# Performance work log

Measured on AMD Instinct MI355X. Metric: run time of the kernel, lower is better.

The kernel has to match this reference:

```python
import jax, jax.numpy as jnp
import numpy as np

N = 50000   # nodes per graph
E = 800000  # edges per graph (even, message() splits in half)
F = 100     # node/edge feature dim (init_count_size / init_emb_size)
D = 64      # hidden_dim3 = rule_graph_dim
W_SCALE = 0.05


def _mlp(x, w1, b1, w2, b2):
    return jax.nn.relu(x @ w1 + b1) @ w2 + b2


def _triple_conv(x, src, dst, ea, lw, lb, l2w, l2b, nn_fn):
    # PyG flow source_to_target: x_j = x[edge_index[0]], x_i = x[edge_index[1]]
    h = ea.shape[0] // 2
    x_j = x[src]
    x_i = x[dst]
    m1 = jax.nn.relu(jnp.concatenate([x_i[:h], ea[:h], x_j[:h]], 1) @ lw + lb)
    m2 = jax.nn.relu(jnp.concatenate([x_j[h:], ea[h:], x_i[h:]], 1) @ l2w + l2b)
    msgs = jnp.concatenate([m1, m2], 0)
    agg = jax.ops.segment_sum(msgs, dst, num_segments=x.shape[0])
    # eps = 0.0 buffer -> out = agg + (1+eps)*x = agg + x
    return nn_fn(agg + x)


def setup_inputs() -> dict:
    key = jax.random.key(0)
    ks = jax.random.split(key, 32)
    inp = {
        'features_1': jax.random.normal(ks[0], (N, F), jnp.float32),
        'edge_index_1': jax.random.randint(ks[1], (2, E), 0, N, jnp.int64 if jax.config.jax_enable_x64 else jnp.int32).astype(jnp.int32),
        'edge_attr_1': jax.random.normal(ks[2], (E, F), jnp.float32),
        'features_2': jax.random.normal(ks[3], (N, F), jnp.float32),
        'edge_index_2': jax.random.randint(ks[4], (2, E), 0, N, jnp.int32),
        'edge_attr_2': jax.random.normal(ks[5], (E, F), jnp.float32),
        'c1_lin_w': jax.random.normal(ks[6], (3 * F, F), jnp.float32) * W_SCALE,
        'c1_lin_b': jax.random.normal(ks[7], (F,), jnp.float32) * W_SCALE,
        'c1_lin2_w': jax.random.normal(ks[8], (3 * F, F), jnp.float32) * W_SCALE,
        'c1_lin2_b': jax.random.normal(ks[9], (F,), jnp.float32) * W_SCALE,
        'mlp1_w1': jax.random.normal(ks[10], (F, F), jnp.float32) * W_SCALE,
        'mlp1_b1': jax.random.normal(ks[11], (F,), jnp.float32) * W_SCALE,
        'mlp1_w2': jax.random.normal(ks[12], (F, F), jnp.float32) * W_SCALE,
        'mlp1_b2': jax.random.normal(ks[13], (F,), jnp.float32) * W_SCALE,
        'c2_lin_w': jax.random.normal(ks[14], (3 * F, F), jnp.float32) * W_SCALE,
        'c2_lin_b': jax.random.normal(ks[15], (F,), jnp.float32) * W_SCALE,
        'c2_lin2_w': jax.random.normal(ks[16], (3 * F, F), jnp.float32) * W_SCALE,
        'c2_lin2_b': jax.random.normal(ks[17], (F,), jnp.float32) * W_SCALE,
        'mlp2_w1': jax.random.normal(ks[18], (F, D), jnp.float32) * W_SCALE,
        'mlp2_b1': jax.random.normal(ks[19], (D,), jnp.float32) * W_SCALE,
        'mlp2_w2': jax.random.normal(ks[20], (D, D), jnp.float32) * W_SCALE,
        'mlp2_b2': jax.random.normal(ks[21], (D,), jnp.float32) * W_SCALE,
    }
    return inp


def reference(features_1, edge_index_1, edge_attr_1,
              features_2, edge_index_2, edge_attr_2,
              c1_lin_w, c1_lin_b, c1_lin2_w, c1_lin2_b,
              mlp1_w1, mlp1_b1, mlp1_w2, mlp1_b2,
              c2_lin_w, c2_lin_b, c2_lin2_w, c2_lin2_b,
              mlp2_w1, mlp2_b1, mlp2_w2, mlp2_b2):

    def conv_pass(x, ei, ea):
        src, dst = ei[0], ei[1]
        x = _triple_conv(x, src, dst, ea, c1_lin_w, c1_lin_b, c1_lin2_w, c1_lin2_b,
                         lambda z: _mlp(z, mlp1_w1, mlp1_b1, mlp1_w2, mlp1_b2))
        x = jax.nn.relu(x)
        x = _triple_conv(x, src, dst, ea, c2_lin_w, c2_lin_b, c2_lin2_w, c2_lin2_b,
                         lambda z: _mlp(z, mlp2_w1, mlp2_b1, mlp2_w2, mlp2_b2))
        return x

    f1 = conv_pass(features_1, edge_index_1, edge_attr_1)  # [N, D]
    f2 = conv_pass(features_2, edge_index_2, edge_attr_2)  # [N, D]
    # global_add_pool with a single batch id -> sum over nodes
    g1 = jnp.sum(f1, axis=0)
    g2 = jnp.sum(f2, axis=0)
    return jnp.stack([g1, g2], 0)  # [2, D]
```

## Files before the change

kernel.cpp:

```cpp
#include <hip/hip_runtime.h>

#define F 100
#define TS 256

typedef __attribute__((ext_vector_type(4))) unsigned short us4;
typedef __attribute__((ext_vector_type(8))) short short8;
typedef __attribute__((ext_vector_type(4))) float f32x4;

static __device__ __forceinline__ unsigned short f2bf(float f) {
    unsigned int u = __float_as_uint(f);
    unsigned int r = (u + 0x7FFF + ((u >> 16) & 1)) >> 16;
    return (unsigned short)r;
}
static __device__ __forceinline__ float bf2f(unsigned short u) {
    return __uint_as_float(((unsigned int)u) << 16);
}

__global__ __launch_bounds__(TS)
void hist2_kernel(const int* __restrict__ dst0, const int* __restrict__ dst1,
                  int h, int E, int N,
                  int* __restrict__ cnt1, int* __restrict__ cnt2)
{
    for (int idx = blockIdx.x * TS + threadIdx.x; idx < 2 * E; idx += gridDim.x * TS) {
        int g = idx >= E;
        int e = idx - g * E;
        int d = (g ? dst1 : dst0)[e];
        atomicAdd((e < h ? cnt1 : cnt2) + g * N + d, 1);
    }
}

__global__ __launch_bounds__(1024)
void scan4_kernel(const int* __restrict__ cnt1, const int* __restrict__ cnt2,
                  int* __restrict__ rp1, int* __restrict__ rp2, int n)
{
    const int which = blockIdx.x;
    const int hf = which >> 1, g = which & 1;
    const int* cnt = (hf ? cnt2 : cnt1) + g * n;
    int* rp = (hf ? rp2 : rp1) + g * (n + 1);
    __shared__ int buf[1024];
    __shared__ int carry_s;
    const int t = threadIdx.x;
    if (t == 0) carry_s = 0;
    __syncthreads();
    for (int base = 0; base < n; base += 8192) {
        int v[8], s = 0;
        #pragma unroll
        for (int j = 0; j < 8; ++j) {
            int idx = base + t * 8 + j;
            int x = (idx < n) ? cnt[idx] : 0;
            v[j] = s; s += x;
        }
        buf[t] = s;
        __syncthreads();
        for (int off = 1; off < 1024; off <<= 1) {
            int y = (t >= off) ? buf[t - off] : 0;
            __syncthreads();
            buf[t] += y;
            __syncthreads();
        }
        int excl = carry_s + buf[t] - s;
        #pragma unroll
        for (int j = 0; j < 8; ++j) {
            int idx = base + t * 8 + j;
            if (idx < n) rp[idx] = excl + v[j];
        }
        __syncthreads();
        if (t == 1023) carry_s += buf[1023];
        __syncthreads();
    }
    if (t == 0) rp[n] = carry_s;
}

__global__ __launch_bounds__(TS)
void scatter2_kernel(const int* __restrict__ src0, const int* __restrict__ dst0,
                     const int* __restrict__ src1, const int* __restrict__ dst1,
                     int h, int E, int N,
                     const int* __restrict__ rp1, const int* __restrict__ rp2,
                     int* __restrict__ cur1, int* __restrict__ cur2,
                     int* __restrict__ perm1, int* __restrict__ perm2,
                     int* __restrict__ es1, int* __restrict__ es2)
{
    for (int idx = blockIdx.x * TS + threadIdx.x; idx < 2 * E; idx += gridDim.x * TS) {
        int g = idx >= E;
        int e = idx - g * E;
        int d = (g ? dst1 : dst0)[e];
        int s = (g ? src1 : src0)[e];
        if (e < h) {
            int p = rp1[g * (N + 1) + d] + atomicAdd(&cur1[g * N + d], 1);
            perm1[g * h + p] = e; es1[g * h + p] = s + g * N;
        } else {
            int p = rp2[g * (N + 1) + d] + atomicAdd(&cur2[g * N + d], 1);
            perm2[g * h + p] = e; es2[g * h + p] = s + g * N;
        }
    }
}

__global__ __launch_bounds__(TS)
void pack_w_kernel(const float* w0, const float* w1, const float* w2, const float* w3,
                   unsigned short* __restrict__ Wp)
{
    int i = blockIdx.x * TS + threadIdx.x;
    if (i >= 12 * 112 * 128) return;
    int s = i / (112 * 128);
    int r = i - s * (112 * 128);
    int c = r >> 7, k = r & 127;
    int wi = s & 3, grp = s >> 2;
    const float* w = (wi == 0) ? w0 : (wi == 1) ? w1 : (wi == 2) ? w2 : w3;
    int off = (grp == 0) ? F : ((grp == 1) ? 0 : 2 * F);
    unsigned short v = 0;
    if (c < 100 && k < 100) v = f2bf(w[(off + k) * F + c]);
    Wp[i] = v;
}

__global__ __launch_bounds__(TS)
void pack_w2_kernel(const float* __restrict__ w, int K, int Nc, int ldb,
                    unsigned short* __restrict__ out)
{
    int i = blockIdx.x * TS + threadIdx.x;
    if (i >= 112 * 128) return;
    int c = i >> 7, k = i & 127;
    unsigned short v = 0;
    if (c < Nc && k < K) v = f2bf(w[k * ldb + c]);
    out[i] = v;
}

__global__ __launch_bounds__(TS)
void pack_x2_kernel(const float* __restrict__ x0, const float* __restrict__ x1,
                    int N, unsigned short* __restrict__ xb)
{
    const size_t total = (size_t)N * 2 * 32;
    for (size_t i = (size_t)blockIdx.x * TS + threadIdx.x; i < total; i += (size_t)gridDim.x * TS) {
        int n = (int)(i >> 5), q = (int)(i & 31);
        int g = n >= N;
        const float* x = g ? x1 : x0;
        int nl = n - g * N;
        us4 o = (us4){0, 0, 0, 0};
        if (q < 25) {
            float4 v = *(const float4*)&x[(size_t)nl * 100 + q * 4];
            o.x = f2bf(v.x); o.y = f2bf(v.y); o.z = f2bf(v.z); o.w = f2bf(v.w);
        }
        *(us4*)&xb[((size_t)n << 7) + q * 4] = o;
    }
}

__global__ __launch_bounds__(TS)
void pack_sum2_f32(const float* __restrict__ agg,
                   const float* __restrict__ x0, const float* __restrict__ x1,
                   int N, unsigned short* __restrict__ Ab)
{
    const size_t total = (size_t)N * 2 * 32;
    for (size_t i = (size_t)blockIdx.x * TS + threadIdx.x; i < total; i += (size_t)gridDim.x * TS) {
        int n = (int)(i >> 5), q = (int)(i & 31);
        int g = n >= N;
        const float* x = g ? x1 : x0;
        int nl = n - g * N;
        us4 o = (us4){0, 0, 0, 0};
        if (q < 25) {
            float4 a = *(const float4*)&agg[(size_t)n * 100 + q * 4];
            float4 v = *(const float4*)&x[(size_t)nl * 100 + q * 4];
            o.x = f2bf(a.x + v.x); o.y = f2bf(a.y + v.y);
            o.z = f2bf(a.z + v.z); o.w = f2bf(a.w + v.w);
        }
        *(us4*)&Ab[((size_t)n << 7) + q * 4] = o;
    }
}

__global__ __launch_bounds__(TS)
void pack_sum_bf16(const float* __restrict__ agg, const unsigned short* __restrict__ xb,
                   int M, unsigned short* __restrict__ Ab)
{
    const size_t total = (size_t)M * 32;
    for (size_t i = (size_t)blockIdx.x * TS + threadIdx.x; i < total; i += (size_t)gridDim.x * TS) {
        int n = (int)(i >> 5), q = (int)(i & 31);
        us4 o = (us4){0, 0, 0, 0};
        if (q < 25) {
            float4 a = *(const float4*)&agg[(size_t)n * 100 + q * 4];
            us4 v = *(const us4*)&xb[((size_t)n << 7) + q * 4];
            o.x = f2bf(a.x + bf2f(v.x)); o.y = f2bf(a.y + bf2f(v.y));
            o.z = f2bf(a.z + bf2f(v.z)); o.w = f2bf(a.w + bf2f(v.w));
        }
        *(us4*)&Ab[((size_t)n << 7) + q * 4] = o;
    }
}

__global__ __launch_bounds__(TS)
void gemm_node_mfma(const unsigned short* __restrict__ xb,
                    const unsigned short* __restrict__ B0, const unsigned short* __restrict__ B1,
                    const unsigned short* __restrict__ B2, const unsigned short* __restrict__ B3,
                    unsigned short* __restrict__ NTb,
                    int M)
{
    const int t = threadIdx.x, lane = t & 63, wv = t >> 6;
    const int rA = lane & 15, kg = lane >> 4;
    const unsigned short* Bp[4] = {B0, B1, B2, B3};
    const int ntiles = (M + 15) >> 4;
    for (int tile = blockIdx.x * 4 + wv; tile < ntiles; tile += gridDim.x * 4) {
        const int base = tile << 4;
        const int arow = min(base + rA, M - 1);
        short8 A[4];
        #pragma unroll
        for (int ks = 0; ks < 4; ++ks)
            A[ks] = *(const short8*)&xb[((size_t)arow << 7) + ks * 32 + kg * 8];
        const int row = base + rA;
        #pragma unroll
        for (int sel = 0; sel < 4; ++sel) {
            const unsigned short* B = Bp[sel];
            f32x4 C[7];
            #pragma unroll
            for (int nf = 0; nf < 7; ++nf) C[nf] = (f32x4){0.f, 0.f, 0.f, 0.f};
            #pragma unroll
            for (int ks = 0; ks < 4; ++ks) {
                #pragma unroll
                for (int nf = 0; nf < 7; ++nf) {
                    short8 Bf = *(const short8*)&B[(size_t)(rA + nf * 16) * 128 + ks * 32 + kg * 8];
                    C[nf] = __builtin_amdgcn_mfma_f32_16x16x32_bf16(Bf, A[ks], C[nf], 0, 0, 0);
                }
            }
            if (row < M) {
                #pragma unroll
                for (int nf = 0; nf < 7; ++nf) {
                    const int cb = nf * 16 + kg * 4;
                    if (cb < 100) {
                        us4 o;
                        o.x = f2bf(C[nf][0]); o.y = f2bf(C[nf][1]);
                        o.z = f2bf(C[nf][2]); o.w = f2bf(C[nf][3]);
                        *(us4*)&NTb[(size_t)row * 400 + sel * 100 + cb] = o;
                    }
                }
            }
        }
    }
}

__global__ __launch_bounds__(TS)
void gemm_edge_quad(const float* __restrict__ ea0, const float* __restrict__ ea1,
                    const int* __restrict__ perm,
                    const unsigned short* __restrict__ W0,
                    const unsigned short* __restrict__ W1,
                    unsigned short* __restrict__ P0,
                    unsigned short* __restrict__ P1,
                    int h)
{
    __shared__ unsigned short sA[2][64][136];
    const int t = threadIdx.x, lane = t & 63, wv = t >> 6;
    const int rA = lane & 15, kg = lane >> 4;
    const int M = 2 * h;
    const int ngrp = M >> 6;
    const int r_loc = t >> 2, sub = t & 3;

    int grp = blockIdx.x;
    if (grp >= ngrp) return;

    {
        const int grow = (grp << 6) + r_loc;
        const int g = grow >= h;
        const int e = perm[grow];
        const float* ea = (g ? ea1 : ea0) + (size_t)e * 100;
        float4 raw[7];
        #pragma unroll
        for (int j = 0; j < 7; ++j) {
            const int q = sub + 4 * j;
            if (q < 25) raw[j] = *(const float4*)&ea[q * 4];
        }
        #pragma unroll
        for (int j = 0; j < 8; ++j) {
            const int q = sub + 4 * j;
            us4 o = (us4){0, 0, 0, 0};
            if (j < 7 && q < 25) {
                o.x = f2bf(raw[j].x); o.y = f2bf(raw[j].y);
                o.z = f2bf(raw[j].z); o.w = f2bf(raw[j].w);
            }
            if (q < 32) *(us4*)&sA[0][r_loc][q * 4] = o;
        }
    }
    __syncthreads();

    int cur = 0;
    while (true) {
        const int nxt = grp + gridDim.x;
        const bool more = nxt < ngrp;

        float4 raw[7];
        if (more) {
            const int grow = (nxt << 6) + r_loc;
            const int g = grow >= h;
            const int e = perm[grow];
            const float* ea = (g ? ea1 : ea0) + (size_t)e * 100;
            #pragma unroll
            for (int j = 0; j < 7; ++j) {
                const int q = sub + 4 * j;
                if (q < 25) raw[j] = *(const float4*)&ea[q * 4];
            }
        }

        {
            const int lrow = wv * 16 + rA;
            short8 A[4];
            #pragma unroll
            for (int ks = 0; ks < 4; ++ks)
                A[ks] = *(const short8*)&sA[cur][lrow][ks * 32 + kg * 8];

            f32x4 C0[7], C1[7];
            #pragma unroll
            for (int nf = 0; nf < 7; ++nf) {
                C0[nf] = (f32x4){0.f, 0.f, 0.f, 0.f};
                C1[nf] = (f32x4){0.f, 0.f, 0.f, 0.f};
            }
            #pragma unroll
            for (int ks = 0; ks < 4; ++ks) {
                #pragma unroll
                for (int nf = 0; nf < 7; ++nf) {
                    short8 B0f = *(const short8*)&W0[(size_t)(rA + nf * 16) * 128 + ks * 32 + kg * 8];
                    C0[nf] = __builtin_amdgcn_mfma_f32_16x16x32_bf16(B0f, A[ks], C0[nf], 0, 0, 0);
                    short8 B1f = *(const short8*)&W1[(size_t)(rA + nf * 16) * 128 + ks * 32 + kg * 8];
                    C1[nf] = __builtin_amdgcn_mfma_f32_16x16x32_bf16(B1f, A[ks], C1[nf], 0, 0, 0);
                }
            }
            const int row = (grp << 6) + lrow;
            #pragma unroll
            for (int nf = 0; nf < 7; ++nf) {
                const int cb = nf * 16 + kg * 4;
                if (cb < 100) {
                    us4 o0, o1;
                    o0.x = f2bf(C0[nf][0]); o0.y = f2bf(C0[nf][1]);
                    o0.z = f2bf(C0[nf][2]); o0.w = f2bf(C0[nf][3]);
                    o1.x = f2bf(C1[nf][0]); o1.y = f2bf(C1[nf][1]);
                    o1.z = f2bf(C1[nf][2]); o1.w = f2bf(C1[nf][3]);
                    *(us4*)&P0[(size_t)row * 100 + cb] = o0;
                    *(us4*)&P1[(size_t)row * 100 + cb] = o1;
                }
            }
        }

        if (!more) break;

        #pragma unroll
        for (int j = 0; j < 8; ++j) {
            const int q = sub + 4 * j;
            us4 o = (us4){0, 0, 0, 0};
            if (j < 7 && q < 25) {
                o.x = f2bf(raw[j].x); o.y = f2bf(raw[j].y);
                o.z = f2bf(raw[j].z); o.w = f2bf(raw[j].w);
            }
            if (q < 32) *(us4*)&sA[cur ^ 1][r_loc][q * 4] = o;
        }
        __syncthreads();
        cur ^= 1; grp = nxt;
    }
}

__global__ __launch_bounds__(TS)
void seg_reduce_both(const unsigned short* __restrict__ PA,
                     const unsigned short* __restrict__ PB,
                     const int* __restrict__ es1, const int* __restrict__ es2,
                     const int* __restrict__ rp1, const int* __restrict__ rp2,
                     const float* __restrict__ cb, const float* __restrict__ cb2,
                     const unsigned short* __restrict__ NTb,
                     float* __restrict__ agg,
                     int N, int h)
{
    const int gid = blockIdx.x * TS + threadIdx.x;
    const int n = gid >> 5, q = gid & 31;
    if (n >= 2 * N || q >= 25) return;
    const int c4 = q * 4;
    const int g = n >= N;
    const int nl = n - g * N;

    float ax = 0.f, ay = 0.f, az = 0.f, aw = 0.f;

    {
        const us4 vd = *(const us4*)&NTb[(size_t)n * 400 + 0 * 100 + c4];
        const float4 bi = *(const float4*)&cb[c4];
        const float dx = bf2f(vd.x) + bi.x, dy = bf2f(vd.y) + bi.y;
        const float dz = bf2f(vd.z) + bi.z, dw = bf2f(vd.w) + bi.w;
        const int* rpg = rp1 + g * (N + 1);
        int p0 = max(rpg[nl], 0) + g * h;
        int p1 = min(rpg[nl + 1], h) + g * h;
        for (int pos = p0; pos < p1; ++pos) {
            const int s = es1[pos];
            const us4 pv = *(const us4*)&PA[(size_t)pos * 100 + c4];
            const us4 vs = *(const us4*)&NTb[(size_t)s * 400 + 1 * 100 + c4];
            ax += fmaxf(bf2f(pv.x) + bf2f(vs.x) + dx, 0.f);
            ay += fmaxf(bf2f(pv.y) + bf2f(vs.y) + dy, 0.f);
            az += fmaxf(bf2f(pv.z) + bf2f(vs.z) + dz, 0.f);
            aw += fmaxf(bf2f(pv.w) + bf2f(vs.w) + dw, 0.f);
        }
    }
    {
        const us4 vd = *(const us4*)&NTb[(size_t)n * 400 + 3 * 100 + c4];
        const float4 bi = *(const float4*)&cb2[c4];
        const float dx = bf2f(vd.x) + bi.x, dy = bf2f(vd.y) + bi.y;
        const float dz = bf2f(vd.z) + bi.z, dw = bf2f(vd.w) + bi.w;
        const int* rpg = rp2 + g * (N + 1);
        int p0 = max(rpg[nl], 0) + g * h;
        int p1 = min(rpg[nl + 1], h) + g * h;
        for (int pos = p0; pos < p1; ++pos) {
            const int s = es2[pos];
            const us4 pv = *(const us4*)&PB[(size_t)pos * 100 + c4];
            const us4 vs = *(const us4*)&NTb[(size_t)s * 400 + 2 * 100 + c4];
            ax += fmaxf(bf2f(pv.x) + bf2f(vs.x) + dx, 0.f);
            ay += fmaxf(bf2f(pv.y) + bf2f(vs.y) + dy, 0.f);
            az += fmaxf(bf2f(pv.z) + bf2f(vs.z) + dz, 0.f);
            aw += fmaxf(bf2f(pv.w) + bf2f(vs.w) + dw, 0.f);
        }
    }
    float* ap = &agg[(size_t)n * 100 + c4];
    ap[0] = ax; ap[1] = ay; ap[2] = az; ap[3] = aw;
}

__global__ __launch_bounds__(TS)
void gemm_mlp_bf16out(const unsigned short* __restrict__ Ab,
                      const unsigned short* __restrict__ Wp,
                      const float* __restrict__ bias,
                      unsigned short* __restrict__ out,
                      int M, int Nc)
{
    const int t = threadIdx.x, lane = t & 63, wv = t >> 6;
    const int rA = lane & 15, kg = lane >> 4;
    const int ntiles = (M + 15) >> 4;
    for (int tile = blockIdx.x * 4 + wv; tile < ntiles; tile += gridDim.x * 4) {
        const int base = tile << 4;
        const int arow = min(base + rA, M - 1);
        f32x4 C[7];
        #pragma unroll
        for (int nf = 0; nf < 7; ++nf) C[nf] = (f32x4){0.f, 0.f, 0.f, 0.f};
        #pragma unroll
        for (int ks = 0; ks < 4; ++ks) {
            short8 A = *(const short8*)&Ab[((size_t)arow << 7) + ks * 32 + kg * 8];
            #pragma unroll
            for (int nf = 0; nf < 7; ++nf) {
                short8 B = *(const short8*)&Wp[(size_t)(rA + nf * 16) * 128 + ks * 32 + kg * 8];
                C[nf] = __builtin_amdgcn_mfma_f32_16x16x32_bf16(B, A, C[nf], 0, 0, 0);
            }
        }
        const int row = base + rA;
        if (row < M) {
            #pragma unroll
            for (int nf = 0; nf < 7; ++nf) {
                const int cb = nf * 16 + kg * 4;
                us4 o = (us4){0, 0, 0, 0};
                if (cb < Nc) {
                    float4 bv = *(const float4*)&bias[cb];
                    o.x = f2bf(fmaxf(C[nf][0] + bv.x, 0.f));
                    o.y = f2bf(fmaxf(C[nf][1] + bv.y, 0.f));
                    o.z = f2bf(fmaxf(C[nf][2] + bv.z, 0.f));
                    o.w = f2bf(fmaxf(C[nf][3] + bv.w, 0.f));
                }
                *(us4*)&out[((size_t)row << 7) + cb] = o;
            }
            *(us4*)&out[((size_t)row << 7) + 112 + kg * 4] = (us4){0, 0, 0, 0};
        }
    }
}

__global__ __launch_bounds__(TS)
void gemm_mlp_f32out(const unsigned short* __restrict__ Ab,
                     const unsigned short* __restrict__ Wp,
                     const float* __restrict__ bias,
                     float* __restrict__ out,
                     int M)
{
    const int t = threadIdx.x, lane = t & 63, wv = t >> 6;
    const int rA = lane & 15, kg = lane >> 4;
    const int ntiles = (M + 15) >> 4;
    for (int tile = blockIdx.x * 4 + wv; tile < ntiles; tile += gridDim.x * 4) {
        const int base = tile << 4;
        const int arow = min(base + rA, M - 1);
        f32x4 C[4];
        #pragma unroll
        for (int nf = 0; nf < 4; ++nf) C[nf] = (f32x4){0.f, 0.f, 0.f, 0.f};
        #pragma unroll
        for (int ks = 0; ks < 2; ++ks) {
            short8 A = *(const short8*)&Ab[((size_t)arow << 7) + ks * 32 + kg * 8];
            #pragma unroll
            for (int nf = 0; nf < 4; ++nf) {
                short8 B = *(const short8*)&Wp[(size_t)(rA + nf * 16) * 128 + ks * 32 + kg * 8];
                C[nf] = __builtin_amdgcn_mfma_f32_16x16x32_bf16(B, A, C[nf], 0, 0, 0);
            }
        }
        const int row = base + rA;
        if (row < M) {
            #pragma unroll
            for (int nf = 0; nf < 4; ++nf) {
                const int cb = nf * 16 + kg * 4;
                float4 bv = *(const float4*)&bias[cb];
                float4 o;
                o.x = C[nf][0] + bv.x; o.y = C[nf][1] + bv.y;
                o.z = C[nf][2] + bv.z; o.w = C[nf][3] + bv.w;
                *(float4*)&out[(size_t)row * 64 + cb] = o;
            }
        }
    }
}

__global__ __launch_bounds__(TS)
void colsum2_kernel(const float* __restrict__ Fm, int N, float* __restrict__ out)
{
    __shared__ float red[4][2][64];
    const int t = threadIdx.x;
    const int c = t & 63, rg = t >> 6;
    float s0 = 0.f, s1 = 0.f;
    const int M = 2 * N;
    for (int r = blockIdx.x * 4 + rg; r < M; r += gridDim.x * 4) {
        float v = Fm[(size_t)r * 64 + c];
        if (r < N) s0 += v; else s1 += v;
    }
    red[rg][0][c] = s0; red[rg][1][c] = s1;
    __syncthreads();
    if (rg == 0) {
        atomicAdd(&out[c],      red[0][0][c] + red[1][0][c] + red[2][0][c] + red[3][0][c]);
        atomicAdd(&out[64 + c], red[0][1][c] + red[1][1][c] + red[2][1][c] + red[3][1][c]);
    }
}

extern "C" void kernel_launch(void* const* d_in, const int* in_sizes, int n_in,
                              void* d_out, int out_size, void* d_ws, size_t ws_size,
                              hipStream_t stream)
{
    const int N = in_sizes[0] / F;
    const int E = in_sizes[1] / 2;
    const int h = E / 2;
    const int N2 = 2 * N, h2 = 2 * h;

    unsigned short* NTb  = (unsigned short*)d_ws;
    float* AGG = (float*)(NTb + (size_t)N2 * 400);
    unsigned short* P1A = (unsigned short*)(AGG + (size_t)N2 * 100);
    unsigned short* P1B = P1A + (size_t)h2 * 100;
    unsigned short* P2A = P1B + (size_t)h2 * 100;
    unsigned short* P2B = P2A + (size_t)h2 * 100;
    unsigned short* xb  = P2B + (size_t)h2 * 100;
    unsigned short* X1b = xb + (size_t)N2 * 128;
    unsigned short* Ab  = X1b + (size_t)N2 * 128;
    unsigned short* Hb  = Ab + (size_t)N2 * 128;
    int* rp1   = (int*)(Hb + (size_t)N2 * 128);
    int* rp2   = rp1 + 2 * (N + 1);
    int* cnt1  = rp2 + 2 * (N + 1);
    int* cnt2  = cnt1 + N2;
    int* perm1 = cnt2 + N2;
    int* perm2 = perm1 + h2;
    int* es1   = perm2 + h2;
    int* es2   = es1 + h2;
    unsigned short* Wp = (unsigned short*)(es2 + h2);
    unsigned short* Wm = Wp + (size_t)12 * 112 * 128;
    float* F2 = AGG;

    const float* x0g0 = (const float*)d_in[0];
    const int*   ei0  = (const int*)d_in[1];
    const float* ea0  = (const float*)d_in[2];
    const float* x0g1 = (const float*)d_in[3];
    const int*   ei1  = (const int*)d_in[4];
    const float* ea1  = (const float*)d_in[5];
    const float* c1w  = (const float*)d_in[6];
    const float* c1b  = (const float*)d_in[7];
    const float* c1w2 = (const float*)d_in[8];
    const float* c1b2 = (const float*)d_in[9];
    const float* m1w1 = (const float*)d_in[10];
    const float* m1b1 = (const float*)d_in[11];
    const float* m1w2 = (const float*)d_in[12];
    const float* m1b2 = (const float*)d_in[13];
    const float* c2w  = (const float*)d_in[14];
    const float* c2b  = (const float*)d_in[15];
    const float* c2w2 = (const float*)d_in[16];
    const float* c2b2 = (const float*)d_in[17];
    const float* m2w1 = (const float*)d_in[18];
    const float* m2b1 = (const float*)d_in[19];
    const float* m2w2 = (const float*)d_in[20];
    const float* m2b2 = (const float*)d_in[21];

    hipMemsetAsync(d_out, 0, (size_t)out_size * sizeof(float), stream);

    const dim3 blk(TS);
    const size_t SL = (size_t)112 * 128;
    pack_w_kernel<<<(12 * 112 * 128 + TS - 1) / TS, blk, 0, stream>>>(c1w, c1w2, c2w, c2w2, Wp);
    pack_w2_kernel<<<56, blk, 0, stream>>>(m1w1, 100, 100, 100, Wm + 0 * SL);
    pack_w2_kernel<<<56, blk, 0, stream>>>(m1w2, 100, 100, 100, Wm + 1 * SL);
    pack_w2_kernel<<<56, blk, 0, stream>>>(m2w1, 100,  64,  64, Wm + 2 * SL);
    pack_w2_kernel<<<56, blk, 0, stream>>>(m2w2,  64,  64,  64, Wm + 3 * SL);

    hipMemsetAsync(cnt1, 0, 2 * (size_t)N2 * sizeof(int), stream);
    hist2_kernel<<<2048, blk, 0, stream>>>(ei0 + E, ei1 + E, h, E, N, cnt1, cnt2);
    scan4_kernel<<<4, 1024, 0, stream>>>(cnt1, cnt2, rp1, rp2, N);
    hipMemsetAsync(cnt1, 0, 2 * (size_t)N2 * sizeof(int), stream);
    scatter2_kernel<<<2048, blk, 0, stream>>>(ei0, ei0 + E, ei1, ei1 + E, h, E, N,
                                              rp1, rp2, cnt1, cnt2, perm1, perm2, es1, es2);
    pack_x2_kernel<<<2048, blk, 0, stream>>>(x0g0, x0g1, N, xb);

    gemm_edge_quad<<<2048, blk, 0, stream>>>(ea0, ea1, perm1,
                                             Wp + 0 * SL, Wp + 2 * SL, P1A, P2A, h);
    gemm_edge_quad<<<2048, blk, 0, stream>>>(ea0, ea1, perm2,
                                             Wp + 1 * SL, Wp + 3 * SL, P1B, P2B, h);

    const int nblkR = (N2 * 32 + TS - 1) / TS;
    for (int conv = 0; conv < 2; ++conv) {
        const float* cb  = conv ? c2b  : c1b;
        const float* cb2 = conv ? c2b2 : c1b2;
        const unsigned short* xin = conv ? X1b : xb;
        const int iw  = conv ? 2 : 0;
        const int iw2 = conv ? 3 : 1;
        const unsigned short* PA = conv ? P2A : P1A;
        const unsigned short* PB = conv ? P2B : P1B;

        gemm_node_mfma<<<2048, blk, 0, stream>>>(xin,
            Wp + (size_t)(4 + iw)  * SL, Wp + (size_t)(8 + iw)  * SL,
            Wp + (size_t)(4 + iw2) * SL, Wp + (size_t)(8 + iw2) * SL,
            NTb, N2);

        seg_reduce_both<<<nblkR, blk, 0, stream>>>(PA, PB, es1, es2, rp1, rp2,
                                                   cb, cb2, NTb, AGG, N, h);

        if (conv == 0) {
            pack_sum2_f32<<<2048, blk, 0, stream>>>(AGG, x0g0, x0g1, N, Ab);
            gemm_mlp_bf16out<<<2048, blk, 0, stream>>>(Ab, Wm + 0 * SL, m1b1, Hb,  N2, 100);
            gemm_mlp_bf16out<<<2048, blk, 0, stream>>>(Hb, Wm + 1 * SL, m1b2, X1b, N2, 100);
        } else {
            pack_sum_bf16<<<2048, blk, 0, stream>>>(AGG, X1b, N2, Ab);
            gemm_mlp_bf16out<<<2048, blk, 0, stream>>>(Ab, Wm + 2 * SL, m2b1, Hb, N2, 64);
            gemm_mlp_f32out<<<2048, blk, 0, stream>>>(Hb, Wm + 3 * SL, m2b2, F2, N2);
        }
    }
    colsum2_kernel<<<512, blk, 0, stream>>>(F2, N, (float*)d_out);
    (void)ws_size; (void)n_in;
}
```

Before: 1.463 ms.

## Fuse edge-attr GEMM with segment reduction per node block using LDS atomics

Replaces the precomputed bf16 edge-projection buffers and the separate segment-reduce kernel with one kernel per conv. Each block owns a range of 40 destination nodes, runs the edge_attr MFMA GEMM on its CSR-sorted edges, adds the source and destination node terms and the bias, applies ReLU, and accumulates into LDS with atomics before writing agg. This removes the large intermediate P buffers and their write/read traffic. In exchange it recomputes the edge GEMM per conv, rereads edge_attr twice, and adds LDS atomic contention plus load imbalance across node blocks.

New measurement: 2.278 ms. 55.7% more time.

```diff
diff --git a/kernel.cpp b/kernel.cpp
--- a/kernel.cpp
+++ b/kernel.cpp
@@ -2,6 +2,7 @@
 
 #define F 100
 #define TS 256
+#define NPB 40
 
 typedef __attribute__((ext_vector_type(4))) unsigned short us4;
 typedef __attribute__((ext_vector_type(8))) short short8;
@@ -78,7 +79,8 @@
                      const int* __restrict__ rp1, const int* __restrict__ rp2,
                      int* __restrict__ cur1, int* __restrict__ cur2,
                      int* __restrict__ perm1, int* __restrict__ perm2,
-                     int* __restrict__ es1, int* __restrict__ es2)
+                     int* __restrict__ es1, int* __restrict__ es2,
+                     int* __restrict__ ds1, int* __restrict__ ds2)
 {
     for (int idx = blockIdx.x * TS + threadIdx.x; idx < 2 * E; idx += gridDim.x * TS) {
         int g = idx >= E;
@@ -87,10 +89,10 @@
         int s = (g ? src1 : src0)[e];
         if (e < h) {
             int p = rp1[g * (N + 1) + d] + atomicAdd(&cur1[g * N + d], 1);
-            perm1[g * h + p] = e; es1[g * h + p] = s + g * N;
+            perm1[g * h + p] = e; es1[g * h + p] = s + g * N; ds1[g * h + p] = d + g * N;
         } else {
             int p = rp2[g * (N + 1) + d] + atomicAdd(&cur2[g * N + d], 1);
-            perm2[g * h + p] = e; es2[g * h + p] = s + g * N;
+            perm2[g * h + p] = e; es2[g * h + p] = s + g * N; ds2[g * h + p] = d + g * N;
         }
     }
 }
@@ -233,179 +235,165 @@
 }
 
 __global__ __launch_bounds__(TS)
-void gemm_edge_quad(const float* __restrict__ ea0, const float* __restrict__ ea1,
-                    const int* __restrict__ perm,
-                    const unsigned short* __restrict__ W0,
-                    const unsigned short* __restrict__ W1,
-                    unsigned short* __restrict__ P0,
-                    unsigned short* __restrict__ P1,
-                    int h)
-{
+void fused_edge_conv(const float* __restrict__ ea0, const float* __restrict__ ea1,
+                     const int* __restrict__ perm1, const int* __restrict__ es1, const int* __restrict__ ds1,
+                     const int* __restrict__ perm2, const int* __restrict__ es2, const int* __restrict__ ds2,
+                     const int* __restrict__ rp1, const int* __restrict__ rp2,
+                     const unsigned short* __restrict__ WA, const unsigned short* __restrict__ WB,
+                     const float* __restrict__ cbA, const float* __restrict__ cbB,
+                     const unsigned short* __restrict__ NTb,
+                     float* __restrict__ agg,
+                     int N, int h, int cpg)
+{
+    __shared__ float aggL[NPB][104];
     __shared__ unsigned short sA[2][64][136];
+
     const int t = threadIdx.x, lane = t & 63, wv = t >> 6;
     const int rA = lane & 15, kg = lane >> 4;
-    const int M = 2 * h;
-    const int ngrp = M >> 6;
     const int r_loc = t >> 2, sub = t & 3;
 
-    int grp = blockIdx.x;
-    if (grp >= ngrp) return;
-
-    {
-        const int grow = (grp << 6) + r_loc;
-        const int g = grow >= h;
-        const int e = perm[grow];
-        const float* ea = (g ? ea1 : ea0) + (size_t)e * 100;
-        float4 raw[7];
-        #pragma unroll
-        for (int j = 0; j < 7; ++j) {
-            const int q = sub + 4 * j;
-            if (q < 25) raw[j] = *(const float4*)&ea[q * 4];
-        }
-        #pragma unroll
-        for (int j = 0; j < 8; ++j) {
-            const int q = sub + 4 * j;
-            us4 o = (us4){0, 0, 0, 0};
-            if (j < 7 && q < 25) {
-                o.x = f2bf(raw[j].x); o.y = f2bf(raw[j].y);
-                o.z = f2bf(raw[j].z); o.w = f2bf(raw[j].w);
-            }
-            if (q < 32) *(us4*)&sA[0][r_loc][q * 4] = o;
-        }
-    }
-    __syncthreads();
-
-    int cur = 0;
-    while (true) {
-        const int nxt = grp + gridDim.x;
-        const bool more = nxt < ngrp;
-
-        float4 raw[7];
-        if (more) {
-            const int grow = (nxt << 6) + r_loc;
-            const int g = grow >= h;
-            const int e = perm[grow];
-            const float* ea = (g ? ea1 : ea0) + (size_t)e * 100;
+    const int b = blockIdx.x;
+    const int g = b >= cpg;
+    const int ci = b - g * cpg;
+    const int n0 = g * N + ci * NPB;
+    const int n1 = min(n0 + NPB, (g + 1) * N);
+    const int nrows = n1 - n0;
+    if (nrows <= 0) return;
+
+    for (int i = t; i < NPB * 104; i += TS) ((float*)aggL)[i] = 0.f;
+
+    const float* eaG = g ? ea1 : ea0;
+
+    #pragma unroll 1
+    for (int ph = 0; ph < 2; ++ph) {
+        const int* rp   = (ph ? rp2 : rp1) + g * (N + 1);
+        const int* perm = ph ? perm2 : perm1;
+        const int* es   = ph ? es2 : es1;
+        const int* ds   = ph ? ds2 : ds1;
+        const unsigned short* W = ph ? WB : WA;
+        const float* cbp = ph ? cbB : cbA;
+        const int seld = ph ? 3 : 0;
+        const int sels = ph ? 2 : 1;
+
+        const int nl0 = n0 - g * N;
+        const int p_lo = rp[nl0] + g * h;
+        const int p_hi = rp[nl0 + nrows] + g * h;
+        if (p_lo >= p_hi) continue;
+
+        float bv[7];
+        #pragma unroll
+        for (int nf = 0; nf < 7; ++nf) {
+            const int c = rA + nf * 16;
+            bv[nf] = (c < 100) ? cbp[c] : 0.f;
+        }
+
+        __syncthreads();
+        {
+            const int pos0 = min(p_lo + r_loc, p_hi - 1);
+            const int e = perm[pos0];
+            const float* er = eaG + (size_t)e * 100;
+            float4 raw[7];
             #pragma unroll
             for (int j = 0; j < 7; ++j) {
                 const int q = sub + 4 * j;
-                if (q < 25) raw[j] = *(const float4*)&ea[q * 4];
-            }
-        }
-
-        {
-            const int lrow = wv * 16 + rA;
-            short8 A[4];
-            #pragma unroll
-            for (int ks = 0; ks < 4; ++ks)
-                A[ks] = *(const short8*)&sA[cur][lrow][ks * 32 + kg * 8];
-
-            f32x4 C0[7], C1[7];
-            #pragma unroll
-            for (int nf = 0; nf < 7; ++nf) {
-                C0[nf] = (f32x4){0.f, 0.f, 0.f, 0.f};
-                C1[nf] = (f32x4){0.f, 0.f, 0.f, 0.f};
-            }
-            #pragma unroll
-            for (int ks = 0; ks < 4; ++ks) {
+                if (q < 25) raw[j] = *(const float4*)&er[q * 4];
+            }
+            #pragma unroll
+            for (int j = 0; j < 8; ++j) {
+                const int q = sub + 4 * j;
+                us4 o = (us4){0, 0, 0, 0};
+                if (j < 7 && q < 25) {
+                    o.x = f2bf(raw[j].x); o.y = f2bf(raw[j].y);
+                    o.z = f2bf(raw[j].z); o.w = f2bf(raw[j].w);
+                }
+                *(us4*)&sA[0][r_loc][q * 4] = o;
+            }
+        }
+        __syncthreads();
+
+        int gb = p_lo, cur = 0;
+        while (true) {
+            const int nb = gb + 64;
+            const bool more = nb < p_hi;
+
+            float4 raw[7];
+            if (more) {
+                const int pos0 = min(nb + r_loc, p_hi - 1);
+                const int e = perm[pos0];
+                const float* er = eaG + (size_t)e * 100;
                 #pragma unroll
-                for (int nf = 0; nf < 7; ++nf) {
-                    short8 B0f = *(const short8*)&W0[(size_t)(rA + nf * 16) * 128 + ks * 32 + kg * 8];
-                    C0[nf] = __builtin_amdgcn_mfma_f32_16x16x32_bf16(B0f, A[ks], C0[nf], 0, 0, 0);
-                    short8 B1f = *(const short8*)&W1[(size_t)(rA + nf * 16) * 128 + ks * 32 + kg * 8];
-                    C1[nf] = __builtin_amdgcn_mfma_f32_16x16x32_bf16(B1f, A[ks], C1[nf], 0, 0, 0);
-                }
-            }
-            const int row = (grp << 6) + lrow;
-            #pragma unroll
-            for (int nf = 0; nf < 7; ++nf) {
-                const int cb = nf * 16 + kg * 4;
-                if (cb < 100) {
-                    us4 o0, o1;
-                    o0.x = f2bf(C0[nf][0]); o0.y = f2bf(C0[nf][1]);
-                    o0.z = f2bf(C0[nf][2]); o0.w = f2bf(C0[nf][3]);
-                    o1.x = f2bf(C1[nf][0]); o1.y = f2bf(C1[nf][1]);
-                    o1.z = f2bf(C1[nf][2]); o1.w = f2bf(C1[nf][3]);
-                    *(us4*)&P0[(size_t)row * 100 + cb] = o0;
-                    *(us4*)&P1[(size_t)row * 100 + cb] = o1;
-                }
-            }
-        }
-
-        if (!more) break;
-
-        #pragma unroll
-        for (int j = 0; j < 8; ++j) {
-            const int q = sub + 4 * j;
-            us4 o = (us4){0, 0, 0, 0};
-            if (j < 7 && q < 25) {
-                o.x = f2bf(raw[j].x); o.y = f2bf(raw[j].y);
-                o.z = f2bf(raw[j].z); o.w = f2bf(raw[j].w);
-            }
-            if (q < 32) *(us4*)&sA[cur ^ 1][r_loc][q * 4] = o;
-        }
-        __syncthreads();
-        cur ^= 1; grp = nxt;
-    }
-}
-
-__global__ __launch_bounds__(TS)
-void seg_reduce_both(const unsigned short* __restrict__ PA,
-                     const unsigned short* __restrict__ PB,
-                     const int* __restrict__ es1, const int* __restrict__ es2,
-                     const int* __restrict__ rp1, const int* __restrict__ rp2,
-                     const float* __restrict__ cb, const float* __restrict__ cb2,
-                     const unsigned short* __restrict__ NTb,
-                     float* __restrict__ agg,
-                     int N, int h)
-{
-    const int gid = blockIdx.x * TS + threadIdx.x;
-    const int n = gid >> 5, q = gid & 31;
-    if (n >= 2 * N || q >= 25) return;
-    const int c4 = q * 4;
-    const int g = n >= N;
-    const int nl = n - g * N;
-
-    float ax = 0.f, ay = 0.f, az = 0.f, aw = 0.f;
-
-    {
-        const us4 vd = *(const us4*)&NTb[(size_t)n * 400 + 0 * 100 + c4];
-        const float4 bi = *(const float4*)&cb[c4];
-        const float dx = bf2f(vd.x) + bi.x, dy = bf2f(vd.y) + bi.y;
-        const float dz = bf2f(vd.z) + bi.z, dw = bf2f(vd.w) + bi.w;
-        const int* rpg = rp1 + g * (N + 1);
-        int p0 = max(rpg[nl], 0) + g * h;
-        int p1 = min(rpg[nl + 1], h) + g * h;
-        for (int pos = p0; pos < p1; ++pos) {
-            const int s = es1[pos];
-            const us4 pv = *(const us4*)&PA[(size_t)pos * 100 + c4];
-            const us4 vs = *(const us4*)&NTb[(size_t)s * 400 + 1 * 100 + c4];
-            ax += fmaxf(bf2f(pv.x) + bf2f(vs.x) + dx, 0.f);
-            ay += fmaxf(bf2f(pv.y) + bf2f(vs.y) + dy, 0.f);
-            az += fmaxf(bf2f(pv.z) + bf2f(vs.z) + dz, 0.f);
-            aw += fmaxf(bf2f(pv.w) + bf2f(vs.w) + dw, 0.f);
-        }
-    }
-    {
-        const us4 vd = *(const us4*)&NTb[(size_t)n * 400 + 3 * 100 + c4];
-        const float4 bi = *(const float4*)&cb2[c4];
-        const float dx = bf2f(vd.x) + bi.x, dy = bf2f(vd.y) + bi.y;
-        const float dz = bf2f(vd.z) + bi.z, dw = bf2f(vd.w) + bi.w;
-        const int* rpg = rp2 + g * (N + 1);
-        int p0 = max(rpg[nl], 0) + g * h;
-        int p1 = min(rpg[nl + 1], h) + g * h;
-        for (int pos = p0; pos < p1; ++pos) {
-            const int s = es2[pos];
-            const us4 pv = *(const us4*)&PB[(size_t)pos * 100 + c4];
-            const us4 vs = *(const us4*)&NTb[(size_t)s * 400 + 2 * 100 + c4];
-            ax += fmaxf(bf2f(pv.x) + bf2f(vs.x) + dx, 0.f);
-            ay += fmaxf(bf2f(pv.y) + bf2f(vs.y) + dy, 0.f);
-            az += fmaxf(bf2f(pv.z) + bf2f(vs.z) + dz, 0.f);
-            aw += fmaxf(bf2f(pv.w) + bf2f(vs.w) + dw, 0.f);
-        }
-    }
-    float* ap = &agg[(size_t)n * 100 + c4];
-    ap[0] = ax; ap[1] = ay; ap[2] = az; ap[3] = aw;
+                for (int j = 0; j < 7; ++j) {
+                    const int q = sub + 4 * j;
+                    if (q < 25) raw[j] = *(const float4*)&er[q * 4];
+                }
+            }
+
+            {
+                const int lrow = wv * 16 + rA;
+                short8 A[4];
+                #pragma unroll
+                for (int ks = 0; ks < 4; ++ks)
+                    A[ks] = *(const short8*)&sA[cur][lrow][ks * 32 + kg * 8];
+
+                f32x4 C[7];
+                #pragma unroll
+                for (int nf = 0; nf < 7; ++nf) C[nf] = (f32x4){0.f, 0.f, 0.f, 0.f};
+                #pragma unroll
+                for (int ks = 0; ks < 4; ++ks) {
+                    #pragma unroll
+                    for (int nf = 0; nf < 7; ++nf) {
+                        short8 Bf = *(const short8*)&W[(size_t)(rA + nf * 16) * 128 + ks * 32 + kg * 8];
+                        C[nf] = __builtin_amdgcn_mfma_f32_16x16x32_bf16(A[ks], Bf, C[nf], 0, 0, 0);
+                    }
+                }
+
+                const int ebase = gb + wv * 16 + kg * 4;
+                #pragma unroll
+                for (int r = 0; r < 4; ++r) {
+                    const int pos = ebase + r;
+                    if (pos < p_hi) {
+                        const int srow = es[pos];
+                        const int drow = ds[pos];
+                        const int dl = drow - n0;
+                        const unsigned short* nts = &NTb[(size_t)srow * 400 + sels * 100];
+                        const unsigned short* ntd = &NTb[(size_t)drow * 400 + seld * 100];
+                        #pragma unroll
+                        for (int nf = 0; nf < 7; ++nf) {
+                            const int c = rA + nf * 16;
+                            if (c < 100) {
+                                float msg = C[nf][r] + bf2f(nts[c]) + bf2f(ntd[c]) + bv[nf];
+                                if (msg > 0.f) atomicAdd(&aggL[dl][c], msg);
+                            }
+                        }
+                    }
+                }
+            }
+
+            if (!more) break;
+
+            #pragma unroll
+            for (int j = 0; j < 8; ++j) {
+                const int q = sub + 4 * j;
+                us4 o = (us4){0, 0, 0, 0};
+                if (j < 7 && q < 25) {
+                    o.x = f2bf(raw[j].x); o.y = f2bf(raw[j].y);
+                    o.z = f2bf(raw[j].z); o.w = f2bf(raw[j].w);
+                }
+                *(us4*)&sA[cur ^ 1][r_loc][q * 4] = o;
+            }
+            __syncthreads();
+            cur ^= 1; gb = nb;
+        }
+    }
+
+    __syncthreads();
+    for (int j = t; j < nrows * 25; j += TS) {
+        const int i = j / 25, q = j - i * 25;
+        float4 v;
+        v.x = aggL[i][q * 4 + 0]; v.y = aggL[i][q * 4 + 1];
+        v.z = aggL[i][q * 4 + 2]; v.w = aggL[i][q * 4 + 3];
+        *(float4*)&agg[(size_t)(n0 + i) * 100 + q * 4] = v;
+    }
 }
 
 __global__ __launch_bounds__(TS)
@@ -524,11 +512,7 @@
 
     unsigned short* NTb  = (unsigned short*)d_ws;
     float* AGG = (float*)(NTb + (size_t)N2 * 400);
-    unsigned short* P1A = (unsigned short*)(AGG + (size_t)N2 * 100);
-    unsigned short* P1B = P1A + (size_t)h2 * 100;
-    unsigned short* P2A = P1B + (size_t)h2 * 100;
-    unsigned short* P2B = P2A + (size_t)h2 * 100;
-    unsigned short* xb  = P2B + (size_t)h2 * 100;
+    unsigned short* xb  = (unsigned short*)(AGG + (size_t)N2 * 100);
     unsigned short* X1b = xb + (size_t)N2 * 128;
     unsigned short* Ab  = X1b + (size_t)N2 * 128;
     unsigned short* Hb  = Ab + (size_t)N2 * 128;
@@ -540,7 +524,9 @@
     int* perm2 = perm1 + h2;
     int* es1   = perm2 + h2;
     int* es2   = es1 + h2;
-    unsigned short* Wp = (unsigned short*)(es2 + h2);
+    int* ds1   = es2 + h2;
+    int* ds2   = ds1 + h2;
+    unsigned short* Wp = (unsigned short*)(ds2 + h2);
     unsigned short* Wm = Wp + (size_t)12 * 112 * 128;
     float* F2 = AGG;
 
@@ -582,31 +568,27 @@
     scan4_kernel<<<4, 1024, 0, stream>>>(cnt1, cnt2, rp1, rp2, N);
     hipMemsetAsync(cnt1, 0, 2 * (size_t)N2 * sizeof(int), stream);
     scatter2_kernel<<<2048, blk, 0, stream>>>(ei0, ei0 + E, ei1, ei1 + E, h, E, N,
-                                              rp1, rp2, cnt1, cnt2, perm1, perm2, es1, es2);
+                                              rp1, rp2, cnt1, cnt2, perm1, perm2,
+                                              es1, es2, ds1, ds2);
     pack_x2_kernel<<<2048, blk, 0, stream>>>(x0g0, x0g1, N, xb);
 
-    gemm_edge_quad<<<2048, blk, 0, stream>>>(ea0, ea1, perm1,
-                                             Wp + 0 * SL, Wp + 2 * SL, P1A, P2A, h);
-    gemm_edge_quad<<<2048, blk, 0, stream>>>(ea0, ea1, perm2,
-                                             Wp + 1 * SL, Wp + 3 * SL, P1B, P2B, h);
-
-    const int nblkR = (N2 * 32 + TS - 1) / TS;
+    const int cpg = (N + NPB - 1) / NPB;
     for (int conv = 0; conv < 2; ++conv) {
         const float* cb  = conv ? c2b  : c1b;
         const float* cb2 = conv ? c2b2 : c1b2;
         const unsigned short* xin = conv ? X1b : xb;
         const int iw  = conv ? 2 : 0;
         const int iw2 = conv ? 3 : 1;
-        const unsigned short* PA = conv ? P2A : P1A;
-        const unsigned short* PB = conv ? P2B : P1B;
 
         gemm_node_mfma<<<2048, blk, 0, stream>>>(xin,
             Wp + (size_t)(4 + iw)  * SL, Wp + (size_t)(8 + iw)  * SL,
             Wp + (size_t)(4 + iw2) * SL, Wp + (size_t)(8 + iw2) * SL,
             NTb, N2);
 
-        seg_reduce_both<<<nblkR, blk, 0, stream>>>(PA, PB, es1, es2, rp1, rp2,
-                                                   cb, cb2, NTb, AGG, N, h);
+        fused_edge_conv<<<2 * cpg, blk, 0, stream>>>(ea0, ea1,
+            perm1, es1, ds1, perm2, es2, ds2, rp1, rp2,
+            Wp + (size_t)iw * SL, Wp + (size_t)iw2 * SL, cb, cb2,
+            NTb, AGG, N, h, cpg);
 
         if (conv == 0) {
             pack_sum2_f32<<<2048, blk, 0, stream>>>(AGG, x0g0, x0g1, N, Ab);
```

## Fuse residual add and bf16 pack into segment reduce; serialize edge GEMM halves

Applied to the files above, without the earlier changes.

The segment-reduce kernel now adds the residual node features (fp32 input or bf16 X1b) and writes the bf16 padded MLP input directly. This removes the separate pack kernels and the fp32 AGG round trip through memory. The edge GEMM also computes its two weight outputs one after another in a non-unrolled loop, which halves live accumulators and should lower register pressure at the cost of less MFMA interleaving. F2 gets its own workspace region.

After: 1.865 ms. 1.27x slower.

```diff
diff --git a/kernel.cpp b/kernel.cpp
--- a/kernel.cpp
+++ b/kernel.cpp
@@ -144,46 +144,6 @@
 }
 
 __global__ __launch_bounds__(TS)
-void pack_sum2_f32(const float* __restrict__ agg,
-                   const float* __restrict__ x0, const float* __restrict__ x1,
-                   int N, unsigned short* __restrict__ Ab)
-{
-    const size_t total = (size_t)N * 2 * 32;
-    for (size_t i = (size_t)blockIdx.x * TS + threadIdx.x; i < total; i += (size_t)gridDim.x * TS) {
-        int n = (int)(i >> 5), q = (int)(i & 31);
-        int g = n >= N;
-        const float* x = g ? x1 : x0;
-        int nl = n - g * N;
-        us4 o = (us4){0, 0, 0, 0};
-        if (q < 25) {
-            float4 a = *(const float4*)&agg[(size_t)n * 100 + q * 4];
-            float4 v = *(const float4*)&x[(size_t)nl * 100 + q * 4];
-            o.x = f2bf(a.x + v.x); o.y = f2bf(a.y + v.y);
-            o.z = f2bf(a.z + v.z); o.w = f2bf(a.w + v.w);
-        }
-        *(us4*)&Ab[((size_t)n << 7) + q * 4] = o;
-    }
-}
-
-__global__ __launch_bounds__(TS)
-void pack_sum_bf16(const float* __restrict__ agg, const unsigned short* __restrict__ xb,
-                   int M, unsigned short* __restrict__ Ab)
-{
-    const size_t total = (size_t)M * 32;
-    for (size_t i = (size_t)blockIdx.x * TS + threadIdx.x; i < total; i += (size_t)gridDim.x * TS) {
-        int n = (int)(i >> 5), q = (int)(i & 31);
-        us4 o = (us4){0, 0, 0, 0};
-        if (q < 25) {
-            float4 a = *(const float4*)&agg[(size_t)n * 100 + q * 4];
-            us4 v = *(const us4*)&xb[((size_t)n << 7) + q * 4];
-            o.x = f2bf(a.x + bf2f(v.x)); o.y = f2bf(a.y + bf2f(v.y));
-            o.z = f2bf(a.z + bf2f(v.z)); o.w = f2bf(a.w + bf2f(v.w));
-        }
-        *(us4*)&Ab[((size_t)n << 7) + q * 4] = o;
-    }
-}
-
-__global__ __launch_bounds__(TS)
 void gemm_node_mfma(const unsigned short* __restrict__ xb,
                     const unsigned short* __restrict__ B0, const unsigned short* __restrict__ B1,
                     const unsigned short* __restrict__ B2, const unsigned short* __restrict__ B3,
@@ -299,35 +259,32 @@
             #pragma unroll
             for (int ks = 0; ks < 4; ++ks)
                 A[ks] = *(const short8*)&sA[cur][lrow][ks * 32 + kg * 8];
-
-            f32x4 C0[7], C1[7];
-            #pragma unroll
-            for (int nf = 0; nf < 7; ++nf) {
-                C0[nf] = (f32x4){0.f, 0.f, 0.f, 0.f};
-                C1[nf] = (f32x4){0.f, 0.f, 0.f, 0.f};
-            }
-            #pragma unroll
-            for (int ks = 0; ks < 4; ++ks) {
+            const int row = (grp << 6) + lrow;
+
+            #pragma unroll 1
+            for (int sel = 0; sel < 2; ++sel) {
+                const unsigned short* W = sel ? W1 : W0;
+                unsigned short* P = sel ? P1 : P0;
+                f32x4 C[7];
+                #pragma unroll
+                for (int nf = 0; nf < 7; ++nf) C[nf] = (f32x4){0.f, 0.f, 0.f, 0.f};
+                #pragma unroll
+                for (int ks = 0; ks < 4; ++ks) {
+                    #pragma unroll
+                    for (int nf = 0; nf < 7; ++nf) {
+                        short8 Bf = *(const short8*)&W[(size_t)(rA + nf * 16) * 128 + ks * 32 + kg * 8];
+                        C[nf] = __builtin_amdgcn_mfma_f32_16x16x32_bf16(Bf, A[ks], C[nf], 0, 0, 0);
+                    }
+                }
                 #pragma unroll
                 for (int nf = 0; nf < 7; ++nf) {
-                    short8 B0f = *(const short8*)&W0[(size_t)(rA + nf * 16) * 128 + ks * 32 + kg * 8];
-                    C0[nf] = __builtin_amdgcn_mfma_f32_16x16x32_bf16(B0f, A[ks], C0[nf], 0, 0, 0);
-                    short8 B1f = *(const short8*)&W1[(size_t)(rA + nf * 16) * 128 + ks * 32 + kg * 8];
-                    C1[nf] = __builtin_amdgcn_mfma_f32_16x16x32_bf16(B1f, A[ks], C1[nf], 0, 0, 0);
-                }
-            }
-            const int row = (grp << 6) + lrow;
-            #pragma unroll
-            for (int nf = 0; nf < 7; ++nf) {
-                const int cb = nf * 16 + kg * 4;
-                if (cb < 100) {
-                    us4 o0, o1;
-                    o0.x = f2bf(C0[nf][0]); o0.y = f2bf(C0[nf][1]);
-                    o0.z = f2bf(C0[nf][2]); o0.w = f2bf(C0[nf][3]);
-                    o1.x = f2bf(C1[nf][0]); o1.y = f2bf(C1[nf][1]);
-                    o1.z = f2bf(C1[nf][2]); o1.w = f2bf(C1[nf][3]);
-                    *(us4*)&P0[(size_t)row * 100 + cb] = o0;
-                    *(us4*)&P1[(size_t)row * 100 + cb] = o1;
+                    const int cb = nf * 16 + kg * 4;
+                    if (cb < 100) {
+                        us4 o;
+                        o.x = f2bf(C[nf][0]); o.y = f2bf(C[nf][1]);
+                        o.z = f2bf(C[nf][2]); o.w = f2bf(C[nf][3]);
+                        *(us4*)&P[(size_t)row * 100 + cb] = o;
+                    }
                 }
             }
         }
@@ -350,19 +307,25 @@
 }
 
 __global__ __launch_bounds__(TS)
-void seg_reduce_both(const unsigned short* __restrict__ PA,
-                     const unsigned short* __restrict__ PB,
-                     const int* __restrict__ es1, const int* __restrict__ es2,
-                     const int* __restrict__ rp1, const int* __restrict__ rp2,
-                     const float* __restrict__ cb, const float* __restrict__ cb2,
-                     const unsigned short* __restrict__ NTb,
-                     float* __restrict__ agg,
-                     int N, int h)
+void seg_reduce_fused(const unsigned short* __restrict__ PA,
+                      const unsigned short* __restrict__ PB,
+                      const int* __restrict__ es1, const int* __restrict__ es2,
+                      const int* __restrict__ rp1, const int* __restrict__ rp2,
+                      const float* __restrict__ cb, const float* __restrict__ cb2,
+                      const unsigned short* __restrict__ NTb,
+                      const float* __restrict__ x0, const float* __restrict__ x1,
+                      const unsigned short* __restrict__ xbin,
+                      unsigned short* __restrict__ Ab,
+                      int N, int h, int mode)
 {
     const int gid = blockIdx.x * TS + threadIdx.x;
     const int n = gid >> 5, q = gid & 31;
-    if (n >= 2 * N || q >= 25) return;
+    if (n >= 2 * N) return;
     const int c4 = q * 4;
+    if (q >= 25) {
+        *(us4*)&Ab[((size_t)n << 7) + c4] = (us4){0, 0, 0, 0};
+        return;
+    }
     const int g = n >= N;
     const int nl = n - g * N;
 
@@ -404,8 +367,19 @@
             aw += fmaxf(bf2f(pv.w) + bf2f(vs.w) + dw, 0.f);
         }
     }
-    float* ap = &agg[(size_t)n * 100 + c4];
-    ap[0] = ax; ap[1] = ay; ap[2] = az; ap[3] = aw;
+
+    float4 xv;
+    if (mode == 0) {
+        const float* x = g ? x1 : x0;
+        xv = *(const float4*)&x[(size_t)nl * 100 + c4];
+    } else {
+        const us4 v = *(const us4*)&xbin[((size_t)n << 7) + c4];
+        xv.x = bf2f(v.x); xv.y = bf2f(v.y); xv.z = bf2f(v.z); xv.w = bf2f(v.w);
+    }
+    us4 o;
+    o.x = f2bf(ax + xv.x); o.y = f2bf(ay + xv.y);
+    o.z = f2bf(az + xv.z); o.w = f2bf(aw + xv.w);
+    *(us4*)&Ab[((size_t)n << 7) + c4] = o;
 }
 
 __global__ __launch_bounds__(TS)
@@ -523,8 +497,7 @@
     const int N2 = 2 * N, h2 = 2 * h;
 
     unsigned short* NTb  = (unsigned short*)d_ws;
-    float* AGG = (float*)(NTb + (size_t)N2 * 400);
-    unsigned short* P1A = (unsigned short*)(AGG + (size_t)N2 * 100);
+    unsigned short* P1A = NTb + (size_t)N2 * 400;
     unsigned short* P1B = P1A + (size_t)h2 * 100;
     unsigned short* P2A = P1B + (size_t)h2 * 100;
     unsigned short* P2B = P2A + (size_t)h2 * 100;
@@ -532,7 +505,8 @@
     unsigned short* X1b = xb + (size_t)N2 * 128;
     unsigned short* Ab  = X1b + (size_t)N2 * 128;
     unsigned short* Hb  = Ab + (size_t)N2 * 128;
-    int* rp1   = (int*)(Hb + (size_t)N2 * 128);
+    float* F2  = (float*)(Hb + (size_t)N2 * 128);
+    int* rp1   = (int*)(F2 + (size_t)N2 * 64);
     int* rp2   = rp1 + 2 * (N + 1);
     int* cnt1  = rp2 + 2 * (N + 1);
     int* cnt2  = cnt1 + N2;
@@ -542,7 +516,6 @@
     int* es2   = es1 + h2;
     unsigned short* Wp = (unsigned short*)(es2 + h2);
     unsigned short* Wm = Wp + (size_t)12 * 112 * 128;
-    float* F2 = AGG;
 
     const float* x0g0 = (const float*)d_in[0];
     const int*   ei0  = (const int*)d_in[1];
@@ -605,15 +578,15 @@
             Wp + (size_t)(4 + iw2) * SL, Wp + (size_t)(8 + iw2) * SL,
             NTb, N2);
 
-        seg_reduce_both<<<nblkR, blk, 0, stream>>>(PA, PB, es1, es2, rp1, rp2,
-                                                   cb, cb2, NTb, AGG, N, h);
+        seg_reduce_fused<<<nblkR, blk, 0, stream>>>(PA, PB, es1, es2, rp1, rp2,
+                                                    cb, cb2, NTb,
+                                                    x0g0, x0g1, X1b, Ab,
+                                                    N, h, conv);
 
         if (conv == 0) {
-            pack_sum2_f32<<<2048, blk, 0, stream>>>(AGG, x0g0, x0g1, N, Ab);
             gemm_mlp_bf16out<<<2048, blk, 0, stream>>>(Ab, Wm + 0 * SL, m1b1, Hb,  N2, 100);
             gemm_mlp_bf16out<<<2048, blk, 0, stream>>>(Hb, Wm + 1 * SL, m1b2, X1b, N2, 100);
         } else {
-            pack_sum_bf16<<<2048, blk, 0, stream>>>(AGG, X1b, N2, Ab);
             gemm_mlp_bf16out<<<2048, blk, 0, stream>>>(Ab, Wm + 2 * SL, m2b1, Hb, N2, 64);
             gemm_mlp_f32out<<<2048, blk, 0, stream>>>(Hb, Wm + 3 * SL, m2b2, F2, N2);
         }
```
